# Optimization experiments

Hardware: AMD Instinct MI355X
Metric: run time of the kernel (lower is better)

## Reference

```python
import jax, jax.numpy as jnp
import numpy as np

ROUTING_ITERS = 3

def squash(v, axis=-1):
    sq = jnp.sum(v * v, axis=axis, keepdims=True)
    scale = sq / (1.0 + sq)
    return scale * v / (jnp.sqrt(sq) + 1e-8)

def setup_inputs() -> dict:
    key = jax.random.key(0)
    k_u, k_w = jax.random.split(key)
    B, IN_CAPS, OUT_CAPS, IN_DIM, OUT_DIM = 256, 1152, 10, 8, 16
    u = jax.random.normal(k_u, (B, IN_CAPS, IN_DIM), dtype=jnp.float32)
    # Xavier uniform over last two dims (out_dim x in_dim matrices)
    bound = float(np.sqrt(6.0 / (OUT_DIM + IN_DIM)))
    W = jax.random.uniform(k_w, (IN_CAPS, OUT_CAPS, OUT_DIM, IN_DIM),
                           dtype=jnp.float32, minval=-bound, maxval=bound)
    return {"u": u, "W": W}

def reference(u, W):
    # u: [b, i, k] (in_dim=k); W: [i, o, d, k] (out_dim=d)
    # u_hat[b,i,o,d] = W[i,o] @ u[b,i]
    u_hat = jnp.einsum('iodk,bik->biod', W, u)  # [B, in_caps, out_caps, out_dim]
    B, I, O, D = u_hat.shape
    b = jnp.zeros((B, I, O), dtype=u_hat.dtype)
    v = None
    for it in range(ROUTING_ITERS):
        c = jax.nn.softmax(b, axis=2)                       # [B, I, O]
        s = jnp.einsum('bio,biod->bod', c, u_hat)           # [B, O, D]
        v = squash(s, axis=-1)                              # [B, O, D]
        if it < ROUTING_ITERS - 1:
            agreement = jnp.einsum('biod,bod->bio', u_hat, v)
            b = b + agreement
    return v
```

## Files before the change

kernel.cpp:

```cpp
#include <hip/hip_runtime.h>
#include <math.h>

#define BB 256
#define IC 1152
#define OC 10
#define OD 16
#define ID 8
#define ODOC (OC*OD)

#define NCHUNK (IC/8)
#define NBG 8
#define UK_THREADS 320

typedef unsigned int   u32;
typedef unsigned short u16;

__device__ __forceinline__ float grp16_sum(float x) {
#pragma unroll
    for (int m = 8; m >= 1; m >>= 1) x += __shfl_xor(x, m, 16);
    return x;
}
__device__ __forceinline__ float grp16_max(float x) {
#pragma unroll
    for (int m = 8; m >= 1; m >>= 1) x = fmaxf(x, __shfl_xor(x, m, 16));
    return x;
}
__device__ __forceinline__ float squash_val(float s) {
    float sq = grp16_sum(s * s);
    return s * (sq / ((1.f + sq) * (sqrtf(sq) + 1e-8f)));
}

__device__ __forceinline__ u32 bf16_rne(float f) {
    u32 x = __float_as_uint(f);
    return (x + 0x7FFFu + ((x >> 16) & 1u)) >> 16;
}
__device__ __forceinline__ u32 pack_bf16x2(float lo, float hi) {
    return bf16_rne(lo) | (bf16_rne(hi) << 16);
}
__device__ __forceinline__ float bf_lo(u32 v) { return __uint_as_float(v << 16); }
__device__ __forceinline__ float bf_hi(u32 v) { return __uint_as_float(v & 0xFFFF0000u); }

__global__ __launch_bounds__(UK_THREADS) void uhat_kernel(const float* __restrict__ u,
                                                          const float* __restrict__ W,
                                                          u16* __restrict__ uhat) {
    __shared__ float us[32][8][ID];

    const int t = threadIdx.x;
    const int chunk = blockIdx.x % NCHUNK;
    const int bg    = blockIdx.x / NCHUNK;
    const int i0 = chunk * 8;

    for (int idx = t; idx < 32 * 8 * ID; idx += UK_THREADS) {
        int bb = idx >> 6, r = idx & 63, il = r >> 3, k = r & 7;
        us[bb][il][k] = u[((size_t)(bb * NBG + bg) * IC + (i0 + il)) * ID + k];
    }
    __syncthreads();

    const int il = t / 40;
    const int r  = t % 40;
    const int o  = r >> 2;
    const int dq = r & 3;
    const int i  = i0 + il;

    float w[4][ID];
    const float* wp = W + (((size_t)i * OC + o) * OD + dq * 4) * ID;
#pragma unroll
    for (int j = 0; j < 4; j++)
#pragma unroll
        for (int k = 0; k < ID; k++) w[j][k] = wp[j * ID + k];

    for (int bb = 0; bb < 32; ++bb) {
        const int b = bb * NBG + bg;
        float a0 = 0.f, a1 = 0.f, a2 = 0.f, a3 = 0.f;
#pragma unroll
        for (int k = 0; k < ID; k++) {
            float uu = us[bb][il][k];
            a0 += w[0][k] * uu;
            a1 += w[1][k] * uu;
            a2 += w[2][k] * uu;
            a3 += w[3][k] * uu;
        }
        uint2 pk = make_uint2(pack_bf16x2(a0, a1), pack_bf16x2(a2, a3));
        *(uint2*)(uhat + ((size_t)b * IC + i) * ODOC + o * OD + dq * 4) = pk;
    }
}

__global__ __launch_bounds__(512) void routing_kernel(const u16* __restrict__ uhat,
                                                      float* __restrict__ out) {
    __shared__ float v_sh[ODOC];
    __shared__ float red[32 * ODOC];

    const int t = threadIdx.x;
    const int b = blockIdx.x;
    const int il   = t >> 4;
    const int slot = t & 15;
    const bool act = slot < OC;

    const u16* ub = uhat + (size_t)b * IC * ODOC;

    float Lreg[36];
#pragma unroll
    for (int j = 0; j < 36; ++j) Lreg[j] = 0.f;

    float sp[OD];
#pragma unroll
    for (int d = 0; d < OD; ++d) sp[d] = 0.f;

#pragma unroll
    for (int step = 0; step < 36; ++step) {
        if (act) {
            const uint4* p = (const uint4*)(ub + (size_t)(step * 32 + il) * ODOC + slot * OD);
            uint4 A = p[0], B = p[1];
            sp[0]  += bf_lo(A.x); sp[1]  += bf_hi(A.x);
            sp[2]  += bf_lo(A.y); sp[3]  += bf_hi(A.y);
            sp[4]  += bf_lo(A.z); sp[5]  += bf_hi(A.z);
            sp[6]  += bf_lo(A.w); sp[7]  += bf_hi(A.w);
            sp[8]  += bf_lo(B.x); sp[9]  += bf_hi(B.x);
            sp[10] += bf_lo(B.y); sp[11] += bf_hi(B.y);
            sp[12] += bf_lo(B.z); sp[13] += bf_hi(B.z);
            sp[14] += bf_lo(B.w); sp[15] += bf_hi(B.w);
        }
    }
    if (act) {
#pragma unroll
        for (int q = 0; q < 4; q++)
            *(float4*)&red[il * ODOC + slot * OD + q * 4] =
                make_float4(sp[q * 4], sp[q * 4 + 1], sp[q * 4 + 2], sp[q * 4 + 3]);
    }
    __syncthreads();
    {
        float s0v = 0.f;
        if (t < ODOC) {
#pragma unroll 8
            for (int j = 0; j < 32; j++) s0v += red[j * ODOC + t];
            s0v *= 0.1f;
        }
        float v0 = squash_val(s0v);
        __syncthreads();
        if (t < ODOC) v_sh[t] = v0;
        __syncthreads();
    }

#pragma unroll 1
    for (int pass = 1; pass <= 2; ++pass) {
        float vr[OD];
        if (act) {
#pragma unroll
            for (int q = 0; q < 4; q++) {
                float4 vq = *(const float4*)&v_sh[slot * OD + q * 4];
                vr[q * 4 + 0] = vq.x; vr[q * 4 + 1] = vq.y;
                vr[q * 4 + 2] = vq.z; vr[q * 4 + 3] = vq.w;
            }
        }
#pragma unroll
        for (int d = 0; d < OD; ++d) sp[d] = 0.f;

#pragma unroll
        for (int step = 0; step < 36; ++step) {
            float uh[OD];
            float a = 0.f;
            if (act) {
                const uint4* p = (const uint4*)(ub + (size_t)(step * 32 + il) * ODOC + slot * OD);
                uint4 A = p[0], B = p[1];
                uh[0]  = bf_lo(A.x); uh[1]  = bf_hi(A.x);
                uh[2]  = bf_lo(A.y); uh[3]  = bf_hi(A.y);
                uh[4]  = bf_lo(A.z); uh[5]  = bf_hi(A.z);
                uh[6]  = bf_lo(A.w); uh[7]  = bf_hi(A.w);
                uh[8]  = bf_lo(B.x); uh[9]  = bf_hi(B.x);
                uh[10] = bf_lo(B.y); uh[11] = bf_hi(B.y);
                uh[12] = bf_lo(B.z); uh[13] = bf_hi(B.z);
                uh[14] = bf_lo(B.w); uh[15] = bf_hi(B.w);
#pragma unroll
                for (int d = 0; d < OD; d++) a += uh[d] * vr[d];
            }
            float Lv = -3.4e38f;
            if (act) { Lreg[step] += a; Lv = Lreg[step]; }
            float mx = grp16_max(Lv);
            float e  = act ? __expf(Lv - mx) : 0.f;
            float S  = grp16_sum(e);
            float c  = e / S;
            if (act) {
#pragma unroll
                for (int d = 0; d < OD; d++) sp[d] += c * uh[d];
            }
        }

        if (act) {
#pragma unroll
            for (int q = 0; q < 4; q++)
                *(float4*)&red[il * ODOC + slot * OD + q * 4] =
                    make_float4(sp[q * 4], sp[q * 4 + 1], sp[q * 4 + 2], sp[q * 4 + 3]);
        }
        __syncthreads();
        float sn = 0.f;
        if (t < ODOC) {
#pragma unroll 8
            for (int j = 0; j < 32; j++) sn += red[j * ODOC + t];
        }
        float vn = squash_val(sn);
        __syncthreads();
        if (pass == 1) {
            if (t < ODOC) v_sh[t] = vn;
            __syncthreads();
        } else {
            if (t < ODOC) out[(size_t)b * ODOC + t] = vn;
        }
    }
}

extern "C" void kernel_launch(void* const* d_in, const int* in_sizes, int n_in,
                              void* d_out, int out_size, void* d_ws, size_t ws_size,
                              hipStream_t stream) {
    const float* u = (const float*)d_in[0];
    const float* W = (const float*)d_in[1];
    float* out = (float*)d_out;

    u16* uhat = (u16*)d_ws;

    hipLaunchKernelGGL(uhat_kernel, dim3(NCHUNK * NBG), dim3(UK_THREADS), 0, stream,
                       u, W, uhat);
    hipLaunchKernelGGL(routing_kernel, dim3(BB), dim3(512), 0, stream,
                       uhat, out);
}
```

Baseline: 103.8 us.

## Fuse first routing sum into uhat kernel and widen routing blocks to 1024 threads

The uhat kernel now accumulates the uniform-coupling first-iteration sum s0 through shared-memory atomics and then global atomics, so the routing kernel no longer makes its first full pass over u_hat. The routing kernel also moves to 1024 threads per batch block, which halves the steps per thread and doubles the shared reduction buffer. The cost is many LDS atomics plus global float atomics and an extra memset. Atomic ordering also makes s0 nondeterministic in its last bits.

```diff
diff --git a/kernel.cpp b/kernel.cpp
--- a/kernel.cpp
+++ b/kernel.cpp
@@ -6,11 +6,14 @@
 #define OC 10
 #define OD 16
 #define ID 8
-#define ODOC (OC*OD)
-
-#define NCHUNK (IC/8)
+#define ODOC 160
+
+#define NCHUNK 144
 #define NBG 8
 #define UK_THREADS 320
+
+#define R_THREADS 1024
+#define R_STEPS (IC/64)
 
 typedef unsigned int   u32;
 typedef unsigned short u16;
@@ -42,8 +45,10 @@
 
 __global__ __launch_bounds__(UK_THREADS) void uhat_kernel(const float* __restrict__ u,
                                                           const float* __restrict__ W,
-                                                          u16* __restrict__ uhat) {
+                                                          u16* __restrict__ uhat,
+                                                          float* __restrict__ s0g) {
     __shared__ float us[32][8][ID];
+    __shared__ float s0_blk[32][ODOC];
 
     const int t = threadIdx.x;
     const int chunk = blockIdx.x % NCHUNK;
@@ -54,6 +59,8 @@
         int bb = idx >> 6, r = idx & 63, il = r >> 3, k = r & 7;
         us[bb][il][k] = u[((size_t)(bb * NBG + bg) * IC + (i0 + il)) * ID + k];
     }
+    for (int idx = t; idx < 32 * ODOC; idx += UK_THREADS)
+        ((float*)s0_blk)[idx] = 0.f;
     __syncthreads();
 
     const int il = t / 40;
@@ -82,13 +89,23 @@
         }
         uint2 pk = make_uint2(pack_bf16x2(a0, a1), pack_bf16x2(a2, a3));
         *(uint2*)(uhat + ((size_t)b * IC + i) * ODOC + o * OD + dq * 4) = pk;
-    }
-}
-
-__global__ __launch_bounds__(512) void routing_kernel(const u16* __restrict__ uhat,
-                                                      float* __restrict__ out) {
+        atomicAdd(&s0_blk[bb][o * OD + dq * 4 + 0], a0);
+        atomicAdd(&s0_blk[bb][o * OD + dq * 4 + 1], a1);
+        atomicAdd(&s0_blk[bb][o * OD + dq * 4 + 2], a2);
+        atomicAdd(&s0_blk[bb][o * OD + dq * 4 + 3], a3);
+    }
+    __syncthreads();
+    for (int idx = t; idx < 32 * ODOC; idx += UK_THREADS) {
+        int bb = idx / ODOC, od = idx % ODOC;
+        atomicAdd(&s0g[(size_t)(bb * NBG + bg) * ODOC + od], s0_blk[bb][od]);
+    }
+}
+
+__global__ __launch_bounds__(R_THREADS, 4) void routing_kernel(const u16* __restrict__ uhat,
+                                                               const float* __restrict__ s0g,
+                                                               float* __restrict__ out) {
     __shared__ float v_sh[ODOC];
-    __shared__ float red[32 * ODOC];
+    __shared__ float red[64 * ODOC];
 
     const int t = threadIdx.x;
     const int b = blockIdx.x;
@@ -96,71 +113,35 @@
     const int slot = t & 15;
     const bool act = slot < OC;
 
+    if (t < ODOC) v_sh[t] = squash_val(s0g[(size_t)b * ODOC + t] * 0.1f);
+    __syncthreads();
+
     const u16* ub = uhat + (size_t)b * IC * ODOC;
 
-    float Lreg[36];
-#pragma unroll
-    for (int j = 0; j < 36; ++j) Lreg[j] = 0.f;
-
-    float sp[OD];
-#pragma unroll
-    for (int d = 0; d < OD; ++d) sp[d] = 0.f;
-
-#pragma unroll
-    for (int step = 0; step < 36; ++step) {
-        if (act) {
-            const uint4* p = (const uint4*)(ub + (size_t)(step * 32 + il) * ODOC + slot * OD);
-            uint4 A = p[0], B = p[1];
-            sp[0]  += bf_lo(A.x); sp[1]  += bf_hi(A.x);
-            sp[2]  += bf_lo(A.y); sp[3]  += bf_hi(A.y);
-            sp[4]  += bf_lo(A.z); sp[5]  += bf_hi(A.z);
-            sp[6]  += bf_lo(A.w); sp[7]  += bf_hi(A.w);
-            sp[8]  += bf_lo(B.x); sp[9]  += bf_hi(B.x);
-            sp[10] += bf_lo(B.y); sp[11] += bf_hi(B.y);
-            sp[12] += bf_lo(B.z); sp[13] += bf_hi(B.z);
-            sp[14] += bf_lo(B.w); sp[15] += bf_hi(B.w);
-        }
-    }
-    if (act) {
-#pragma unroll
-        for (int q = 0; q < 4; q++)
-            *(float4*)&red[il * ODOC + slot * OD + q * 4] =
-                make_float4(sp[q * 4], sp[q * 4 + 1], sp[q * 4 + 2], sp[q * 4 + 3]);
-    }
-    __syncthreads();
-    {
-        float s0v = 0.f;
-        if (t < ODOC) {
-#pragma unroll 8
-            for (int j = 0; j < 32; j++) s0v += red[j * ODOC + t];
-            s0v *= 0.1f;
-        }
-        float v0 = squash_val(s0v);
-        __syncthreads();
-        if (t < ODOC) v_sh[t] = v0;
-        __syncthreads();
-    }
+    float Lreg[R_STEPS];
+#pragma unroll
+    for (int j = 0; j < R_STEPS; ++j) Lreg[j] = 0.f;
 
 #pragma unroll 1
     for (int pass = 1; pass <= 2; ++pass) {
         float vr[OD];
-        if (act) {
-#pragma unroll
-            for (int q = 0; q < 4; q++) {
-                float4 vq = *(const float4*)&v_sh[slot * OD + q * 4];
-                vr[q * 4 + 0] = vq.x; vr[q * 4 + 1] = vq.y;
-                vr[q * 4 + 2] = vq.z; vr[q * 4 + 3] = vq.w;
-            }
-        }
+#pragma unroll
+        for (int q = 0; q < 4; q++) {
+            float4 vq = *(const float4*)&v_sh[slot * OD + q * 4];
+            vr[q * 4 + 0] = vq.x; vr[q * 4 + 1] = vq.y;
+            vr[q * 4 + 2] = vq.z; vr[q * 4 + 3] = vq.w;
+        }
+        float sp[OD];
 #pragma unroll
         for (int d = 0; d < OD; ++d) sp[d] = 0.f;
 
 #pragma unroll
-        for (int step = 0; step < 36; ++step) {
+        for (int step = 0; step < R_STEPS; ++step) {
+            const int i = step * 64 + il;
             float uh[OD];
             float a = 0.f;
             if (act) {
-                const uint4* p = (const uint4*)(ub + (size_t)(step * 32 + il) * ODOC + slot * OD);
+                const uint4* p = (const uint4*)(ub + (size_t)i * ODOC + slot * OD);
                 uint4 A = p[0], B = p[1];
                 uh[0]  = bf_lo(A.x); uh[1]  = bf_hi(A.x);
                 uh[2]  = bf_lo(A.y); uh[3]  = bf_hi(A.y);
@@ -195,7 +176,7 @@
         float sn = 0.f;
         if (t < ODOC) {
 #pragma unroll 8
-            for (int j = 0; j < 32; j++) sn += red[j * ODOC + t];
+            for (int j = 0; j < 64; j++) sn += red[j * ODOC + t];
         }
         float vn = squash_val(sn);
         __syncthreads();
@@ -215,10 +196,13 @@
     const float* W = (const float*)d_in[1];
     float* out = (float*)d_out;
 
-    u16* uhat = (u16*)d_ws;
-
+    const size_t uhat_bytes = (size_t)BB * IC * ODOC * sizeof(u16);
+    u16*   uhat = (u16*)d_ws;
+    float* s0g  = (float*)((char*)d_ws + uhat_bytes);
+
+    hipMemsetAsync(s0g, 0, (size_t)BB * ODOC * sizeof(float), stream);
     hipLaunchKernelGGL(uhat_kernel, dim3(NCHUNK * NBG), dim3(UK_THREADS), 0, stream,
-                       u, W, uhat);
-    hipLaunchKernelGGL(routing_kernel, dim3(BB), dim3(512), 0, stream,
-                       uhat, out);
-}
+                       u, W, uhat, s0g);
+    hipLaunchKernelGGL(routing_kernel, dim3(BB), dim3(R_THREADS), 0, stream,
+                       uhat, s0g, out);
+}
```

New measurement: 323.6 us. 212% more time.
